# Kernel tuning notes

Measured on AMD Instinct MI355X. Metric: run time of the kernel, lower is better.

Reference implementation:

```python
import jax, jax.numpy as jnp
import numpy as np

B, S, DH, DF, DM = 32, 2048, 1024, 1024, 512


def setup_inputs() -> dict:
    key = jax.random.key(0)
    ks = jax.random.split(key, 7)
    s_h = 1.0 / np.sqrt(DH)
    s_f = 1.0 / np.sqrt(DF)
    s_m = 1.0 / np.sqrt(DM)
    return {
        "hidden_states": jax.random.normal(ks[0], (B, DH), jnp.float32),
        "feats": jax.random.normal(ks[1], (B, S, DF), jnp.float32),
        "W1h": jax.random.uniform(ks[2], (DM, DH), jnp.float32, -s_h, s_h),
        "b1h": jax.random.uniform(ks[3], (DM,), jnp.float32, -s_h, s_h),
        "W1f": jax.random.uniform(ks[4], (DM, DF), jnp.float32, -s_f, s_f),
        "b1f": jax.random.uniform(ks[5], (DM,), jnp.float32, -s_f, s_f),
        "w2": jax.random.uniform(ks[6], (DM,), jnp.float32, -s_m, s_m),
    }


def reference(hidden_states, feats, W1h, b1h, W1f, b1f, w2):
    # additive (Bahdanau) attention, single feature stream
    emb_h = hidden_states @ W1h.T + b1h                     # [B, DM]
    emb_f = jnp.einsum('bsd,md->bsm', feats, W1f) + b1f      # [B, S, DM]
    emb = jnp.tanh(emb_h[:, None, :] + emb_f)                # [B, S, DM]
    logits = jnp.einsum('bsm,m->bs', emb, w2)                # [B, S]
    probs = jax.nn.softmax(logits, axis=-1)                  # [B, S]
    context = jnp.einsum('bs,bsd->bd', probs, feats)         # [B, DF]
    # torch: cat(context, dim=1) -> [B, DF]; stack(probs, dim=1) -> [B, 1, S]
    return context, probs[:, None, :]
```

## Files before the change

### kernel.cpp

```cpp
#include <hip/hip_runtime.h>
#include <hip/hip_bf16.h>
#include <cstdint>
#include <cstddef>

#define B_   32
#define S_   2048
#define DH_  1024
#define DF_  1024
#define DM_  512
#define MTOT (B_ * S_)

typedef __attribute__((ext_vector_type(8))) short bf16x8;
typedef __attribute__((ext_vector_type(4))) float f32x4;

#define AS1 __attribute__((address_space(1)))
#define AS3 __attribute__((address_space(3)))

static __device__ __forceinline__ void load_lds16(const void* g, void* l) {
    __builtin_amdgcn_global_load_lds((const AS1 unsigned*)g, (AS3 unsigned*)l,
                                     16, 0, 0);
}

static __device__ __forceinline__ unsigned pack_rhu(float a, float b) {
    unsigned ua = (__float_as_uint(a) + 0x8000u) >> 16;
    unsigned ub = (__float_as_uint(b) + 0x8000u) & 0xFFFF0000u;
    return ua | ub;
}

static __device__ __forceinline__ float tanh_fast(float x) {
    float e = __expf(2.0f * x);
    return 1.0f - 2.0f / (e + 1.0f);
}

__global__ __launch_bounds__(256) void k_embh(
    const float* __restrict__ hidden, const float* __restrict__ W1h,
    const float* __restrict__ b1h, const float* __restrict__ b1f,
    float* __restrict__ embh)
{
    int b  = blockIdx.x;
    int mg = blockIdx.y;
    int t  = threadIdx.x;
    int m  = mg * 64 + (t >> 2);
    int kp = (t & 3) * 256;
    const float4* h4 = (const float4*)(hidden + (size_t)b * DH_ + kp);
    const float4* w4 = (const float4*)(W1h + (size_t)m * DH_ + kp);
    float s = 0.0f;
    #pragma unroll 8
    for (int i = 0; i < 64; ++i) {
        float4 a = h4[i];
        float4 w = w4[i];
        s += a.x * w.x + a.y * w.y + a.z * w.z + a.w * w.w;
    }
    s += __shfl_xor(s, 1);
    s += __shfl_xor(s, 2);
    if ((t & 3) == 0)
        embh[b * DM_ + m] = s + b1h[m] + b1f[m];
}

__global__ __launch_bounds__(256) void k_cvt(
    const float* __restrict__ src, unsigned short* __restrict__ dst)
{
    size_t i = (size_t)blockIdx.x * 256 + threadIdx.x;
    float4 a = ((const float4*)src)[2 * i];
    float4 b = ((const float4*)src)[2 * i + 1];
    uint4 r;
    r.x = pack_rhu(a.x, a.y);
    r.y = pack_rhu(a.z, a.w);
    r.z = pack_rhu(b.x, b.y);
    r.w = pack_rhu(b.z, b.w);
    ((uint4*)dst)[i] = r;
}

__global__ __launch_bounds__(256) void k_gemm_bf(
    const unsigned short* __restrict__ fb, const unsigned short* __restrict__ wb,
    const float* __restrict__ embh, const float* __restrict__ w2,
    float* __restrict__ plog)
{
    __shared__ bf16x8 As[4 * 128];
    __shared__ bf16x8 Bs[4 * 128];

    const int t    = threadIdx.x;
    const int lane = t & 63;
    const int w    = t >> 6;
    const int wm   = w >> 1;
    const int wn   = w & 1;
    const int quad = lane >> 4;
    const int l16  = lane & 15;

    const int blk   = blockIdx.x;
    const int panel = blk >> 5;
    const int sub   = blk & 31;
    const int bx    = sub >> 3;
    const int by    = panel * 8 + (sub & 7);

    const unsigned short* aG0 = fb + ((size_t)(by * 128) + lane) * DF_ + w * 8;
    const unsigned short* aG1 = aG0 + (size_t)64 * DF_;
    const unsigned short* bG0 = wb + ((size_t)(bx * 128) + lane) * DF_ + w * 8;
    const unsigned short* bG1 = bG0 + (size_t)64 * DF_;
    bf16x8* ldsA0 = &As[w * 128];
    bf16x8* ldsA1 = &As[w * 128 + 64];
    bf16x8* ldsB0 = &Bs[w * 128];
    bf16x8* ldsB1 = &Bs[w * 128 + 64];

    f32x4 acc[4][4];
    const f32x4 zero = {0.0f, 0.0f, 0.0f, 0.0f};
    #pragma unroll
    for (int i = 0; i < 4; ++i)
        #pragma unroll
        for (int j = 0; j < 4; ++j) acc[i][j] = zero;

    for (int kt = 0; kt < DF_ / 32; ++kt) {
        __syncthreads();
        load_lds16(aG0 + kt * 32, ldsA0);
        load_lds16(aG1 + kt * 32, ldsA1);
        load_lds16(bG0 + kt * 32, ldsB0);
        load_lds16(bG1 + kt * 32, ldsB1);
        __syncthreads();

        bf16x8 af[4], bfr[4];
        #pragma unroll
        for (int mi = 0; mi < 4; ++mi)
            af[mi] = As[quad * 128 + wm * 64 + mi * 16 + l16];
        #pragma unroll
        for (int nj = 0; nj < 4; ++nj)
            bfr[nj] = Bs[quad * 128 + wn * 64 + nj * 16 + l16];

        #pragma unroll
        for (int mi = 0; mi < 4; ++mi)
            #pragma unroll
            for (int nj = 0; nj < 4; ++nj)
                acc[mi][nj] = __builtin_amdgcn_mfma_f32_16x16x32_bf16(
                    af[mi], bfr[nj], acc[mi][nj], 0, 0, 0);
    }

    const int bIdx = by >> 4;
    float ew[4], wv[4];
    #pragma unroll
    for (int nj = 0; nj < 4; ++nj) {
        int c = bx * 128 + wn * 64 + nj * 16 + l16;
        ew[nj] = embh[bIdx * DM_ + c];
        wv[nj] = w2[c];
    }
    float* plw = plog + (size_t)(bx * 2 + wn) * MTOT + bIdx * S_;
    #pragma unroll
    for (int mi = 0; mi < 4; ++mi) {
        #pragma unroll
        for (int reg = 0; reg < 4; ++reg) {
            float p = 0.0f;
            #pragma unroll
            for (int nj = 0; nj < 4; ++nj)
                p += tanh_fast(acc[mi][nj][reg] + ew[nj]) * wv[nj];
            p += __shfl_xor(p, 1);
            p += __shfl_xor(p, 2);
            p += __shfl_xor(p, 4);
            p += __shfl_xor(p, 8);
            if (l16 == 0) {
                int rowl = wm * 64 + mi * 16 + quad * 4 + reg;
                int s = (by * 128 + rowl) & (S_ - 1);
                plw[s] = p;
            }
        }
    }
}

__global__ __launch_bounds__(256) void k_gemm_f32(
    const float* __restrict__ feats, const unsigned short* __restrict__ w1fb,
    const float* __restrict__ embh, const float* __restrict__ w2,
    float* __restrict__ plog)
{
    __shared__ bf16x8 As[4 * 128];
    __shared__ bf16x8 Bs[4 * 128];

    const int t    = threadIdx.x;
    const int lane = t & 63;
    const int w    = t >> 6;
    const int wm   = w >> 1;
    const int wn   = w & 1;
    const int quad = lane >> 4;
    const int l16  = lane & 15;
    const int blk   = blockIdx.x;
    const int panel = blk >> 5;
    const int sub   = blk & 31;
    const int bx    = sub >> 3;
    const int by    = panel * 8 + (sub & 7);

    const int sRow = t >> 1;
    const int sK   = (t & 1) * 16;
    const int c0   = sK >> 3;
    const float*          aG = feats + (size_t)(by * 128 + sRow) * DF_ + sK;
    const unsigned short* bG = w1fb  + (size_t)(bx * 128 + sRow) * DF_ + sK;

    f32x4 acc[4][4];
    const f32x4 zero = {0.0f, 0.0f, 0.0f, 0.0f};
    #pragma unroll
    for (int i = 0; i < 4; ++i)
        #pragma unroll
        for (int j = 0; j < 4; ++j) acc[i][j] = zero;

    for (int kt = 0; kt < DF_ / 32; ++kt) {
        float4 a0 = *(const float4*)(aG + kt * 32);
        float4 a1 = *(const float4*)(aG + kt * 32 + 4);
        float4 a2 = *(const float4*)(aG + kt * 32 + 8);
        float4 a3 = *(const float4*)(aG + kt * 32 + 12);
        uint4  b0 = *(const uint4*)(bG + kt * 32);
        uint4  b1 = *(const uint4*)(bG + kt * 32 + 8);

        __syncthreads();

        union { unsigned u[4]; bf16x8 v; } pa;
        pa.u[0] = pack_rhu(a0.x, a0.y);
        pa.u[1] = pack_rhu(a0.z, a0.w);
        pa.u[2] = pack_rhu(a1.x, a1.y);
        pa.u[3] = pack_rhu(a1.z, a1.w);
        As[c0 * 128 + sRow] = pa.v;
        pa.u[0] = pack_rhu(a2.x, a2.y);
        pa.u[1] = pack_rhu(a2.z, a2.w);
        pa.u[2] = pack_rhu(a3.x, a3.y);
        pa.u[3] = pack_rhu(a3.z, a3.w);
        As[(c0 + 1) * 128 + sRow] = pa.v;

        union { uint4 q; bf16x8 v; } pb;
        pb.q = b0;
        Bs[c0 * 128 + sRow] = pb.v;
        pb.q = b1;
        Bs[(c0 + 1) * 128 + sRow] = pb.v;

        __syncthreads();

        bf16x8 af[4], bfr[4];
        #pragma unroll
        for (int mi = 0; mi < 4; ++mi)
            af[mi] = As[quad * 128 + wm * 64 + mi * 16 + l16];
        #pragma unroll
        for (int nj = 0; nj < 4; ++nj)
            bfr[nj] = Bs[quad * 128 + wn * 64 + nj * 16 + l16];

        #pragma unroll
        for (int mi = 0; mi < 4; ++mi)
            #pragma unroll
            for (int nj = 0; nj < 4; ++nj)
                acc[mi][nj] = __builtin_amdgcn_mfma_f32_16x16x32_bf16(
                    af[mi], bfr[nj], acc[mi][nj], 0, 0, 0);
    }

    const int bIdx = by >> 4;
    float ew[4], wv[4];
    #pragma unroll
    for (int nj = 0; nj < 4; ++nj) {
        int c = bx * 128 + wn * 64 + nj * 16 + l16;
        ew[nj] = embh[bIdx * DM_ + c];
        wv[nj] = w2[c];
    }
    float* plw = plog + (size_t)(bx * 2 + wn) * MTOT + bIdx * S_;
    #pragma unroll
    for (int mi = 0; mi < 4; ++mi) {
        #pragma unroll
        for (int reg = 0; reg < 4; ++reg) {
            float p = 0.0f;
            #pragma unroll
            for (int nj = 0; nj < 4; ++nj)
                p += tanh_fast(acc[mi][nj][reg] + ew[nj]) * wv[nj];
            p += __shfl_xor(p, 1);
            p += __shfl_xor(p, 2);
            p += __shfl_xor(p, 4);
            p += __shfl_xor(p, 8);
            if (l16 == 0) {
                int rowl = wm * 64 + mi * 16 + quad * 4 + reg;
                int s = (by * 128 + rowl) & (S_ - 1);
                plw[s] = p;
            }
        }
    }
}

__global__ __launch_bounds__(256) void k_softmax(
    const float* __restrict__ plog, float* __restrict__ probs_out)
{
    int b = blockIdx.x;
    int t = threadIdx.x;
    float l[8];
    #pragma unroll
    for (int i = 0; i < 8; ++i) {
        int s = t + i * 256;
        float sum = 0.0f;
        #pragma unroll
        for (int p = 0; p < 8; ++p)
            sum += plog[(size_t)p * MTOT + b * S_ + s];
        l[i] = sum;
    }
    float mx = l[0];
    #pragma unroll
    for (int i = 1; i < 8; ++i) mx = fmaxf(mx, l[i]);
    #pragma unroll
    for (int off = 1; off < 64; off <<= 1) mx = fmaxf(mx, __shfl_xor(mx, off));
    __shared__ float redm[4];
    __shared__ float reds[4];
    int wid = t >> 6;
    if ((t & 63) == 0) redm[wid] = mx;
    __syncthreads();
    mx = fmaxf(fmaxf(redm[0], redm[1]), fmaxf(redm[2], redm[3]));

    float e[8];
    float es = 0.0f;
    #pragma unroll
    for (int i = 0; i < 8; ++i) {
        e[i] = __expf(l[i] - mx);
        es += e[i];
    }
    #pragma unroll
    for (int off = 1; off < 64; off <<= 1) es += __shfl_xor(es, off);
    if ((t & 63) == 0) reds[wid] = es;
    __syncthreads();
    es = reds[0] + reds[1] + reds[2] + reds[3];
    float inv = 1.0f / es;
    #pragma unroll
    for (int i = 0; i < 8; ++i)
        probs_out[b * S_ + t + i * 256] = e[i] * inv;
}

__global__ __launch_bounds__(256) void k_context_bf(
    const unsigned short* __restrict__ fb, const float* __restrict__ probs,
    float* __restrict__ ctxp)
{
    int dp = blockIdx.x * 256 + threadIdx.x;
    int b  = blockIdx.y;
    int z  = blockIdx.z;
    const unsigned* f  = (const unsigned*)(fb + ((size_t)b * S_ + z * 256) * DF_) + dp;
    const float*    pr = probs + b * S_ + z * 256;
    float a0 = 0.0f, a1 = 0.0f;
    #pragma unroll 4
    for (int i = 0; i < 256; ++i) {
        unsigned v = f[(size_t)i * (DF_ / 2)];
        float lo = __uint_as_float(v << 16);
        float hi = __uint_as_float(v & 0xFFFF0000u);
        float p = pr[i];
        a0 += p * lo;
        a1 += p * hi;
    }
    float2* o = (float2*)(ctxp + ((size_t)z * B_ + b) * DF_) + dp;
    *o = make_float2(a0, a1);
}

__global__ __launch_bounds__(256) void k_context_f32(
    const float* __restrict__ feats, const float* __restrict__ probs,
    float* __restrict__ ctxp)
{
    int d  = blockIdx.x * 256 + threadIdx.x;
    int b  = blockIdx.y;
    int z  = blockIdx.z;
    const float* f  = feats + ((size_t)b * S_ + z * 256) * DF_ + d;
    const float* pr = probs + b * S_ + z * 256;
    float acc = 0.0f;
    #pragma unroll 4
    for (int i = 0; i < 256; ++i)
        acc += pr[i] * f[(size_t)i * DF_];
    ctxp[((size_t)z * B_ + b) * DF_ + d] = acc;
}

__global__ __launch_bounds__(256) void k_ctx_red(
    const float* __restrict__ ctxp, float* __restrict__ ctx)
{
    int i = blockIdx.x * 256 + threadIdx.x;
    float s = 0.0f;
    #pragma unroll
    for (int z = 0; z < 8; ++z)
        s += ctxp[(size_t)z * B_ * DF_ + i];
    ctx[i] = s;
}

extern "C" void kernel_launch(void* const* d_in, const int* in_sizes, int n_in,
                              void* d_out, int out_size, void* d_ws, size_t ws_size,
                              hipStream_t stream)
{
    const float* hidden = (const float*)d_in[0];
    const float* feats  = (const float*)d_in[1];
    const float* W1h    = (const float*)d_in[2];
    const float* b1h    = (const float*)d_in[3];
    const float* W1f    = (const float*)d_in[4];
    const float* b1f    = (const float*)d_in[5];
    const float* w2     = (const float*)d_in[6];

    float* out   = (float*)d_out;
    float* ctx   = out;
    float* probs = out + B_ * DF_;

    char* ws = (char*)d_ws;
    float*          embh  = (float*)ws;
    unsigned short* w1fb  = (unsigned short*)(ws + (64 << 10));
    float*          plog  = (float*)(ws + (64 << 10) + (1 << 20));
    float*          ctxp  = (float*)(ws + (64 << 10) + (3 << 20));
    unsigned short* featb = (unsigned short*)(ws + (8 << 20));

    const bool big_ws = ws_size >= ((size_t)8 << 20) + ((size_t)B_ * S_ * DF_ * 2);

    k_embh<<<dim3(B_, DM_ / 64), 256, 0, stream>>>(hidden, W1h, b1h, b1f, embh);
    k_cvt<<<dim3((DM_ * DF_ / 8) / 256), 256, 0, stream>>>(W1f, w1fb);

    if (big_ws) {
        k_cvt<<<dim3(((size_t)MTOT * DF_ / 8) / 256), 256, 0, stream>>>(feats, featb);
        k_gemm_bf<<<dim3((MTOT / 128) * (DM_ / 128)), 256, 0, stream>>>(
            featb, w1fb, embh, w2, plog);
        k_softmax<<<dim3(B_), 256, 0, stream>>>(plog, probs);
        k_context_bf<<<dim3(DF_ / 512, B_, 8), 256, 0, stream>>>(featb, probs, ctxp);
    } else {
        k_gemm_f32<<<dim3((MTOT / 128) * (DM_ / 128)), 256, 0, stream>>>(
            feats, w1fb, embh, w2, plog);
        k_softmax<<<dim3(B_), 256, 0, stream>>>(plog, probs);
        k_context_f32<<<dim3(DF_ / 256, B_, 8), 256, 0, stream>>>(feats, probs, ctxp);
    }
    k_ctx_red<<<dim3(B_ * DF_ / 256), 256, 0, stream>>>(ctxp, ctx);
}
```

Baseline: 574.7 us.

## Double-buffer LDS tiles in bf16 GEMM and split context reduction finer

The bf16 GEMM now keeps two LDS tile buffers. It prefetches the next K-slice with global_load_lds while the MFMAs consume the current one, which removes one of the two barriers per iteration. The goal is to hide global-to-LDS latency behind compute, at the cost of twice the LDS footprint. The bf16 context kernel also splits the sequence into 16 chunks of 128 instead of 8 chunks of 256, which gives more blocks for parallelism. The partial-sum reducer is templated on the chunk count to match.

```diff
diff --git a/kernel.cpp b/kernel.cpp
--- a/kernel.cpp
+++ b/kernel.cpp
@@ -9,6 +9,7 @@
 #define DF_  1024
 #define DM_  512
 #define MTOT (B_ * S_)
+#define NK   (DF_ / 32)
 
 typedef __attribute__((ext_vector_type(8))) short bf16x8;
 typedef __attribute__((ext_vector_type(4))) float f32x4;
@@ -76,8 +77,8 @@
     const float* __restrict__ embh, const float* __restrict__ w2,
     float* __restrict__ plog)
 {
-    __shared__ bf16x8 As[4 * 128];
-    __shared__ bf16x8 Bs[4 * 128];
+    __shared__ bf16x8 As[2][4 * 128];
+    __shared__ bf16x8 Bs[2][4 * 128];
 
     const int t    = threadIdx.x;
     const int lane = t & 63;
@@ -97,10 +98,6 @@
     const unsigned short* aG1 = aG0 + (size_t)64 * DF_;
     const unsigned short* bG0 = wb + ((size_t)(bx * 128) + lane) * DF_ + w * 8;
     const unsigned short* bG1 = bG0 + (size_t)64 * DF_;
-    bf16x8* ldsA0 = &As[w * 128];
-    bf16x8* ldsA1 = &As[w * 128 + 64];
-    bf16x8* ldsB0 = &Bs[w * 128];
-    bf16x8* ldsB1 = &Bs[w * 128 + 64];
 
     f32x4 acc[4][4];
     const f32x4 zero = {0.0f, 0.0f, 0.0f, 0.0f};
@@ -109,21 +106,32 @@
         #pragma unroll
         for (int j = 0; j < 4; ++j) acc[i][j] = zero;
 
-    for (int kt = 0; kt < DF_ / 32; ++kt) {
+    load_lds16(aG0, &As[0][w * 128]);
+    load_lds16(aG1, &As[0][w * 128 + 64]);
+    load_lds16(bG0, &Bs[0][w * 128]);
+    load_lds16(bG1, &Bs[0][w * 128 + 64]);
+
+    #pragma unroll 2
+    for (int kt = 0; kt < NK; ++kt) {
+        const int cur = kt & 1;
+        const int nxt = cur ^ 1;
+
         __syncthreads();
-        load_lds16(aG0 + kt * 32, ldsA0);
-        load_lds16(aG1 + kt * 32, ldsA1);
-        load_lds16(bG0 + kt * 32, ldsB0);
-        load_lds16(bG1 + kt * 32, ldsB1);
-        __syncthreads();
+
+        if (kt + 1 < NK) {
+            load_lds16(aG0 + (kt + 1) * 32, &As[nxt][w * 128]);
+            load_lds16(aG1 + (kt + 1) * 32, &As[nxt][w * 128 + 64]);
+            load_lds16(bG0 + (kt + 1) * 32, &Bs[nxt][w * 128]);
+            load_lds16(bG1 + (kt + 1) * 32, &Bs[nxt][w * 128 + 64]);
+        }
 
         bf16x8 af[4], bfr[4];
         #pragma unroll
         for (int mi = 0; mi < 4; ++mi)
-            af[mi] = As[quad * 128 + wm * 64 + mi * 16 + l16];
+            af[mi] = As[cur][quad * 128 + wm * 64 + mi * 16 + l16];
         #pragma unroll
         for (int nj = 0; nj < 4; ++nj)
-            bfr[nj] = Bs[quad * 128 + wn * 64 + nj * 16 + l16];
+            bfr[nj] = Bs[cur][quad * 128 + wn * 64 + nj * 16 + l16];
 
         #pragma unroll
         for (int mi = 0; mi < 4; ++mi)
@@ -197,7 +205,7 @@
         #pragma unroll
         for (int j = 0; j < 4; ++j) acc[i][j] = zero;
 
-    for (int kt = 0; kt < DF_ / 32; ++kt) {
+    for (int kt = 0; kt < NK; ++kt) {
         float4 a0 = *(const float4*)(aG + kt * 32);
         float4 a1 = *(const float4*)(aG + kt * 32 + 4);
         float4 a2 = *(const float4*)(aG + kt * 32 + 8);
@@ -325,11 +333,11 @@
     int dp = blockIdx.x * 256 + threadIdx.x;
     int b  = blockIdx.y;
     int z  = blockIdx.z;
-    const unsigned* f  = (const unsigned*)(fb + ((size_t)b * S_ + z * 256) * DF_) + dp;
-    const float*    pr = probs + b * S_ + z * 256;
+    const unsigned* f  = (const unsigned*)(fb + ((size_t)b * S_ + z * 128) * DF_) + dp;
+    const float*    pr = probs + b * S_ + z * 128;
     float a0 = 0.0f, a1 = 0.0f;
     #pragma unroll 4
-    for (int i = 0; i < 256; ++i) {
+    for (int i = 0; i < 128; ++i) {
         unsigned v = f[(size_t)i * (DF_ / 2)];
         float lo = __uint_as_float(v << 16);
         float hi = __uint_as_float(v & 0xFFFF0000u);
@@ -357,13 +365,14 @@
     ctxp[((size_t)z * B_ + b) * DF_ + d] = acc;
 }
 
+template <int NZ>
 __global__ __launch_bounds__(256) void k_ctx_red(
     const float* __restrict__ ctxp, float* __restrict__ ctx)
 {
     int i = blockIdx.x * 256 + threadIdx.x;
     float s = 0.0f;
     #pragma unroll
-    for (int z = 0; z < 8; ++z)
+    for (int z = 0; z < NZ; ++z)
         s += ctxp[(size_t)z * B_ * DF_ + i];
     ctx[i] = s;
 }
@@ -401,12 +410,13 @@
         k_gemm_bf<<<dim3((MTOT / 128) * (DM_ / 128)), 256, 0, stream>>>(
             featb, w1fb, embh, w2, plog);
         k_softmax<<<dim3(B_), 256, 0, stream>>>(plog, probs);
-        k_context_bf<<<dim3(DF_ / 512, B_, 8), 256, 0, stream>>>(featb, probs, ctxp);
+        k_context_bf<<<dim3(DF_ / 512, B_, 16), 256, 0, stream>>>(featb, probs, ctxp);
+        k_ctx_red<16><<<dim3(B_ * DF_ / 256), 256, 0, stream>>>(ctxp, ctx);
     } else {
         k_gemm_f32<<<dim3((MTOT / 128) * (DM_ / 128)), 256, 0, stream>>>(
             feats, w1fb, embh, w2, plog);
         k_softmax<<<dim3(B_), 256, 0, stream>>>(plog, probs);
         k_context_f32<<<dim3(DF_ / 256, B_, 8), 256, 0, stream>>>(feats, probs, ctxp);
-    }
-    k_ctx_red<<<dim3(B_ * DF_ / 256), 256, 0, stream>>>(ctxp, ctx);
-}
+        k_ctx_red<8><<<dim3(B_ * DF_ / 256), 256, 0, stream>>>(ctxp, ctx);
+    }
+}
```

New measurement: 585.1 us. About the same (+1.8%).
